# Kernel tuning notes

Hardware: AMD Instinct MI355X
Metric: run time of the kernel (lower is better)

## Reference

```python
import jax, jax.numpy as jnp
import numpy as np

EPS = 1e-5  # torch BatchNorm1d default eps
O, T, D, H1, H2 = 8, 4, 256, 64, 32


def setup_inputs() -> dict:
    key = jax.random.key(0)
    ks = jax.random.split(key, 8)
    B = 65536
    feature = jax.random.normal(ks[0], (B, D), dtype=jnp.float32)
    treatment = jax.random.randint(ks[1], (B,), 0, T, dtype=jnp.int64)
    s1 = 1.0 / np.sqrt(D)
    s2 = 1.0 / np.sqrt(H1)
    s3 = 1.0 / np.sqrt(H2)
    params = {
        # per (outcome, treatment) expert MLP weights
        'W1': jax.random.uniform(ks[2], (O, T, D, H1), jnp.float32, -s1, s1),
        'b1': jnp.zeros((O, T, H1), jnp.float32),
        'g1': jnp.ones((O, T, H1), jnp.float32),   # BN1 gamma
        'be1': jnp.zeros((O, T, H1), jnp.float32),  # BN1 beta
        'm1': jnp.zeros((O, T, H1), jnp.float32),   # BN1 running mean
        'v1': jnp.ones((O, T, H1), jnp.float32),    # BN1 running var
        'W2': jax.random.uniform(ks[3], (O, T, H1, H2), jnp.float32, -s2, s2),
        'b2': jnp.zeros((O, T, H2), jnp.float32),
        'g2': jnp.ones((O, T, H2), jnp.float32),
        'be2': jnp.zeros((O, T, H2), jnp.float32),
        'm2': jnp.zeros((O, T, H2), jnp.float32),
        'v2': jnp.ones((O, T, H2), jnp.float32),
        'W3': jax.random.uniform(ks[4], (O, T, H2), jnp.float32, -s3, s3),  # final Linear(32,1), squeezed
        'b3': jnp.zeros((O, T), jnp.float32),
    }
    return {'feature': feature, 'treatment': treatment, **params}


def _tlearner_fwd(x, t, W1, b1, g1, be1, m1, v1, W2, b2, g2, be2, m2, v2, W3, b3):
    # Dense evaluation of every (outcome, treatment) expert, then per-row
    # selection by treatment id. Equivalent (in eval mode: BN uses running
    # stats, dropout off) to the masked dispatch of the original module.
    h = jnp.einsum('bd,otdh->both', x, W1) + b1          # [B,O,T,H1]
    h = jax.nn.relu(h)
    h = (h - m1) * jax.lax.rsqrt(v1 + EPS) * g1 + be1    # BN1 (eval)
    h = jnp.einsum('both,othk->botk', h, W2) + b2        # [B,O,T,H2]
    h = jax.nn.relu(h)
    h = (h - m2) * jax.lax.rsqrt(v2 + EPS) * g2 + be2    # BN2 (eval)
    out = jnp.einsum('botk,otk->bot', h, W3) + b3        # [B,O,T]
    idx = t.astype(jnp.int32)[:, None, None]             # [B,1,1]
    return jnp.take_along_axis(out, jnp.broadcast_to(idx, (out.shape[0], O, 1)), axis=2)[..., 0]  # [B,O]


def reference(feature, treatment, W1, b1, g1, be1, m1, v1, W2, b2, g2, be2, m2, v2, W3, b3):
    return _tlearner_fwd(feature, treatment, W1, b1, g1, be1, m1, v1,
                         W2, b2, g2, be2, m2, v2, W3, b3)
```

## Files before the change

kernel.cpp:

```cpp
#include <hip/hip_runtime.h>
#include <cstdint>

typedef short bf16x8 __attribute__((ext_vector_type(8)));
typedef float f32x4 __attribute__((ext_vector_type(4)));

#define NO 8
#define NT 4
#define ND 256
#define NH1 64
#define NH2 32
#define BM 64
#define BNEPS 1e-5f

__device__ __forceinline__ unsigned bfpack2(float a, float b) {
    unsigned ua = __float_as_uint(a), ub = __float_as_uint(b);
    ua = (ua + 0x7FFFu + ((ua >> 16) & 1u)) >> 16;
    ub = (ub + 0x7FFFu + ((ub >> 16) & 1u)) >> 16;
    return ua | (ub << 16);
}


__global__ void k_hist_prep(const int* __restrict__ trt, int* __restrict__ ws, int B,
                            const float* __restrict__ W1, const float* __restrict__ W2,
                            const float* __restrict__ b1, const float* __restrict__ g1,
                            const float* __restrict__ be1, const float* __restrict__ m1,
                            const float* __restrict__ v1,
                            const float* __restrict__ b2, const float* __restrict__ g2,
                            const float* __restrict__ be2, const float* __restrict__ m2,
                            const float* __restrict__ v2, const float* __restrict__ W3,
                            unsigned* __restrict__ W1T4, unsigned* __restrict__ W2T4,
                            float* __restrict__ P1, float* __restrict__ P2) {
    const int bid = blockIdx.x, tid = threadIdx.x;
    if (bid < 256) {
        __shared__ int loc[NT];
        if (tid < NT) loc[tid] = 0;
        __syncthreads();
        const int i = bid * 256 + tid;
        if (i < B) atomicAdd(&loc[trt[i] & 3], 1);
        __syncthreads();
        if (tid < NT) atomicAdd(&ws[tid], loc[tid]);
    } else if (bid < 512) {
        const int gi = (bid - 256) * 256 + tid;
        const int lane = gi & 63, nt = (gi >> 6) & 31, c = (gi >> 11) & 7, t = gi >> 14;
        const int n16 = lane & 15, kg = lane >> 4;
        const int n = nt * 16 + n16, o = n >> 6, h = n & 63;
        const int k0 = c * 32 + kg * 8;
        const float* src = W1 + ((size_t)(o * NT + t) * ND + k0) * NH1 + h;
        float v[8];
#pragma unroll
        for (int j = 0; j < 8; ++j) v[j] = src[(size_t)j * NH1];
        uint4 q;
        q.x = bfpack2(v[0], v[1]); q.y = bfpack2(v[2], v[3]);
        q.z = bfpack2(v[4], v[5]); q.w = bfpack2(v[6], v[7]);
        ((uint4*)W1T4)[gi] = q;
    } else if (bid < 544) {
        const int gi = (bid - 512) * 256 + tid;
        const int m16 = gi & 15, kg = (gi >> 4) & 3, ks = (gi >> 6) & 1,
                  kt = (gi >> 7) & 1, o = (gi >> 8) & 7, t = gi >> 11;
        const int k2 = kt * 16 + m16, hb = ks * 32 + kg * 8;
        const float* src = W2 + ((size_t)(o * NT + t) * NH1 + hb) * NH2 + k2;
        float v[8];
#pragma unroll
        for (int j = 0; j < 8; ++j) v[j] = src[(size_t)j * NH2];
        uint4 q;
        q.x = bfpack2(v[0], v[1]); q.y = bfpack2(v[2], v[3]);
        q.z = bfpack2(v[4], v[5]); q.w = bfpack2(v[6], v[7]);
        ((uint4*)W2T4)[gi] = q;
    } else if (bid < 552) {
        const int gi = (bid - 544) * 256 + tid;
        const int t = gi >> 9, n = gi & 511;
        const int o = n >> 6, h = n & 63;
        const int idx = (o * NT + t) * NH1 + h;
        const float sc = g1[idx] * rsqrtf(v1[idx] + BNEPS);
        P1[gi] = sc;
        P1[2048 + gi] = be1[idx] - m1[idx] * sc;
        P1[4096 + gi] = b1[idx];
    } else {
        const int gi = (bid - 552) * 256 + tid;
        const int t = gi >> 8, q = gi & 255;
        const int o = q >> 5, k2 = q & 31;
        const int idx = (o * NT + t) * NH2 + k2;
        const float s = g2[idx] * rsqrtf(v2[idx] + BNEPS);
        const float w3 = W3[idx];
        P2[gi] = s * w3;
        P2[1024 + gi] = (be2[idx] - m2[idx] * s) * w3;
        P2[2048 + gi] = b2[idx];
    }
}

__global__ void k_scatter(const int* __restrict__ trt, int* __restrict__ ws,
                          int* __restrict__ rperm, int B) {
    __shared__ int loc[NT], gb[NT];
    const int tid = threadIdx.x;
    if (tid < NT) loc[tid] = 0;
    __syncthreads();
    const int i = blockIdx.x * blockDim.x + tid;
    int tt = 0, pos = 0;
    if (i < B) { tt = trt[i] & 3; pos = atomicAdd(&loc[tt], 1); }
    __syncthreads();
    if (tid < NT) {
        const int c0 = ws[0], c1 = ws[1], c2 = ws[2];
        const int q0 = (c0 + 63) & ~63, q1 = (c1 + 63) & ~63, q2 = (c2 + 63) & ~63;
        const int eb = tid == 0 ? 0 : tid == 1 ? q0 : tid == 2 ? q0 + q1 : q0 + q1 + q2;
        gb[tid] = eb + atomicAdd(&ws[4 + tid], loc[tid]);
    }
    __syncthreads();
    if (i < B) rperm[gb[tt] + pos] = i;
}

__global__ __launch_bounds__(512, 2) void k_main(
    const float* __restrict__ X, const int* __restrict__ ws, const int* __restrict__ rperm,
    const char* __restrict__ W1T, const char* __restrict__ W2T,
    const float* __restrict__ P1, const float* __restrict__ P2,
    const float* __restrict__ pb3, float* __restrict__ out)
{
    const int c0 = ws[0], c1 = ws[1], c2 = ws[2], c3 = ws[3];
    const int q0 = (c0 + 63) & ~63, q1 = (c1 + 63) & ~63, q2 = (c2 + 63) & ~63;
    const int e0 = q0, e1 = q0 + q1, e2 = e1 + q2, e3 = e2 + ((c3 + 63) & ~63);
    const int m0 = blockIdx.x * BM;
    if (m0 >= e3) return;
    const int t = (m0 >= e0) + (m0 >= e1) + (m0 >= e2);

    const int tid = threadIdx.x;
    const int w = tid >> 6;
    const int l = tid & 63;

    __shared__ __align__(16) char LDS[65536];

    const int rid_l = rperm[m0 + l];

#pragma unroll
    for (int j = 0; j < 8; ++j) {
        const int r = w * 8 + j;
        const int rr = __shfl(rid_l, r);
        const int rrow = rr < 0 ? 0 : rr;
        const float4 xv = *(const float4*)(X + (size_t)rrow * ND + l * 4);
        uint2 pk;
        pk.x = bfpack2(xv.x, xv.y);
        pk.y = bfpack2(xv.z, xv.w);
        *(uint2*)(LDS + r * 512 + ((l * 8) ^ ((r & 7) << 4))) = pk;
    }

    f32x4 acc[4][4];
#pragma unroll
    for (int jn = 0; jn < 4; ++jn)
#pragma unroll
        for (int rt = 0; rt < 4; ++rt) acc[jn][rt] = (f32x4){0.f, 0.f, 0.f, 0.f};

    const char* W1Tw = W1T + (size_t)t * 262144 + (w * 4) * 1024 + l * 16;
    const int ln4 = (l >> 4) * 4;

    __syncthreads();

#pragma unroll
    for (int c = 0; c < 8; ++c) {
        bf16x8 aA[4];
#pragma unroll
        for (int jn = 0; jn < 4; ++jn)
            aA[jn] = *(const bf16x8*)(W1Tw + c * 32768 + jn * 1024);
#pragma unroll
        for (int rt = 0; rt < 4; ++rt) {
            const int r = rt * 16 + (l & 15);
            const bf16x8 bX = *(const bf16x8*)(LDS + r * 512 +
                                               ((c * 64 + (l >> 4) * 16) ^ ((r & 7) << 4)));
#pragma unroll
            for (int jn = 0; jn < 4; ++jn)
                acc[jn][rt] = __builtin_amdgcn_mfma_f32_16x16x32_bf16(aA[jn], bX, acc[jn][rt], 0, 0, 0);
        }
    }
    __syncthreads();

#pragma unroll
    for (int jn = 0; jn < 4; ++jn) {
        const int n0 = (w * 4 + jn) * 16 + ln4;
        const int p = t * 512 + n0;
        const float4 scv = *(const float4*)(P1 + p);
        const float4 shv = *(const float4*)(P1 + 2048 + p);
        const float4 bbv = *(const float4*)(P1 + 4096 + p);
#pragma unroll
        for (int rt = 0; rt < 4; ++rt) {
            const int r = rt * 16 + (l & 15);
            const f32x4 a = acc[jn][rt];
            const float z0 = fmaf(fmaxf(a[0] + bbv.x, 0.f), scv.x, shv.x);
            const float z1 = fmaf(fmaxf(a[1] + bbv.y, 0.f), scv.y, shv.y);
            const float z2 = fmaf(fmaxf(a[2] + bbv.z, 0.f), scv.z, shv.z);
            const float z3 = fmaf(fmaxf(a[3] + bbv.w, 0.f), scv.w, shv.w);
            uint2 pk;
            pk.x = bfpack2(z0, z1); pk.y = bfpack2(z2, z3);
            *(uint2*)(LDS + r * 1024 + (((unsigned)(n0 * 2)) ^ (unsigned)((r & 7) << 4))) = pk;
        }
    }

    bf16x8 aW[2][2];
#pragma unroll
    for (int kt = 0; kt < 2; ++kt)
#pragma unroll
        for (int ks = 0; ks < 2; ++ks)
            aW[kt][ks] = *(const bf16x8*)(W2T +
                ((((size_t)t * NO + w) * 2 + kt) * 2 + ks) * 1024 + l * 16);

    f32x4 acc2[2][4];
#pragma unroll
    for (int kt = 0; kt < 2; ++kt)
#pragma unroll
        for (int rt2 = 0; rt2 < 4; ++rt2) acc2[kt][rt2] = (f32x4){0.f, 0.f, 0.f, 0.f};

#pragma unroll
    for (int rt2 = 0; rt2 < 4; ++rt2) {
        const int r = rt2 * 16 + (l & 15);
        const unsigned swz = (unsigned)((r & 7) << 4);
#pragma unroll
        for (int ks = 0; ks < 2; ++ks) {
            const int n8 = w * 64 + ks * 32 + (l >> 4) * 8;
            const bf16x8 bH = *(const bf16x8*)(LDS + r * 1024 + (((unsigned)(n8 * 2)) ^ swz));
#pragma unroll
            for (int kt = 0; kt < 2; ++kt)
                acc2[kt][rt2] = __builtin_amdgcn_mfma_f32_16x16x32_bf16(aW[kt][ks], bH, acc2[kt][rt2], 0, 0, 0);
        }
    }

    float pr[4];
#pragma unroll
    for (int rt2 = 0; rt2 < 4; ++rt2) pr[rt2] = 0.f;

#pragma unroll
    for (int kt = 0; kt < 2; ++kt) {
        const int q3 = w * 32 + kt * 16 + ln4;
        const int p3 = t * 256 + q3;
        const float4 A3 = *(const float4*)(P2 + p3);
        const float4 C3 = *(const float4*)(P2 + 1024 + p3);
        const float4 bb = *(const float4*)(P2 + 2048 + p3);
#pragma unroll
        for (int rt2 = 0; rt2 < 4; ++rt2) {
            const f32x4 a = acc2[kt][rt2];
            float s = fmaf(fmaxf(a[0] + bb.x, 0.f), A3.x, C3.x);
            s = fmaf(fmaxf(a[1] + bb.y, 0.f), A3.y, s + C3.y);
            s = fmaf(fmaxf(a[2] + bb.z, 0.f), A3.z, s + C3.z);
            s = fmaf(fmaxf(a[3] + bb.w, 0.f), A3.w, s + C3.w);
            pr[rt2] += s;
        }
    }
#pragma unroll
    for (int rt2 = 0; rt2 < 4; ++rt2) {
        float v = pr[rt2];
        v += __shfl_xor(v, 16);
        v += __shfl_xor(v, 32);
        pr[rt2] = v;
    }

    const int sel = l >> 4;
    const float v = sel == 0 ? pr[0] : sel == 1 ? pr[1] : sel == 2 ? pr[2] : pr[3];
    if (rid_l >= 0) out[(size_t)rid_l * NO + w] = v + pb3[w * NT + t];
}

extern "C" void kernel_launch(void* const* d_in, const int* in_sizes, int n_in,
                              void* d_out, int out_size, void* d_ws, size_t ws_size,
                              hipStream_t stream) {
    const float* X   = (const float*)d_in[0];
    const int* trt   = (const int*)d_in[1];
    const float* W1  = (const float*)d_in[2];
    const float* b1  = (const float*)d_in[3];
    const float* g1  = (const float*)d_in[4];
    const float* be1 = (const float*)d_in[5];
    const float* m1  = (const float*)d_in[6];
    const float* v1  = (const float*)d_in[7];
    const float* W2  = (const float*)d_in[8];
    const float* b2  = (const float*)d_in[9];
    const float* g2  = (const float*)d_in[10];
    const float* be2 = (const float*)d_in[11];
    const float* m2  = (const float*)d_in[12];
    const float* v2  = (const float*)d_in[13];
    const float* W3  = (const float*)d_in[14];
    const float* b3  = (const float*)d_in[15];
    float* out = (float*)d_out;

    const int B = in_sizes[1];
    const int permCap = B + 4 * BM;
    int* wsi   = (int*)d_ws;
    int* rperm = wsi + 16;
    char* wsb  = (char*)d_ws;
    size_t off = (64 + (size_t)permCap * 4 + 15) & ~(size_t)15;
    char* W1T = wsb + off;
    char* W2T = W1T + 1048576;
    float* P1 = (float*)(W2T + 131072);
    float* P2 = P1 + 6144;

    hipMemsetAsync(wsi, 0, 64, stream);
    hipMemsetAsync(rperm, 0xFF, (size_t)permCap * 4, stream);

    k_hist_prep<<<556, 256, 0, stream>>>(trt, wsi, B, W1, W2,
                                         b1, g1, be1, m1, v1,
                                         b2, g2, be2, m2, v2, W3,
                                         (unsigned*)W1T, (unsigned*)W2T, P1, P2);
    k_scatter<<<(B + 255) / 256, 256, 0, stream>>>(trt, wsi, rperm, B);

    const int gx = (B + 63) / 64 + 4;
    k_main<<<gx, 512, 0, stream>>>(X, wsi, rperm, W1T, W2T, P1, P2, b3, out);
}
```

Before: 63.18 us.

## Halve row tile to 32, raise occupancy, use hardware bf16 pack

Shrinks the per-block row tile from 64 to 32 rows, which halves LDS use and accumulator registers. This allows launch bounds of 4 blocks per CU instead of 2, and the treatment-group padding and grid size are adjusted to 32-row alignment. The software bf16 rounding is replaced with the v_cvt_pk_bf16_f32 instruction, and the layer-1 bias is folded into the accumulator initialisation. The trade-off is that each block still streams the full per-treatment W1 slice, so total weight traffic from cache roughly doubles.

```diff
diff --git a/kernel.cpp b/kernel.cpp
--- a/kernel.cpp
+++ b/kernel.cpp
@@ -9,7 +9,7 @@
 #define ND 256
 #define NH1 64
 #define NH2 32
-#define BM 64
+#define BM 32
 #define BNEPS 1e-5f
 
 __device__ __forceinline__ unsigned bfpack2(float a, float b) {
@@ -17,6 +17,12 @@
     ua = (ua + 0x7FFFu + ((ua >> 16) & 1u)) >> 16;
     ub = (ub + 0x7FFFu + ((ub >> 16) & 1u)) >> 16;
     return ua | (ub << 16);
+}
+
+__device__ __forceinline__ unsigned cvtpk(float lo, float hi) {
+    unsigned r;
+    asm("v_cvt_pk_bf16_f32 %0, %1, %2" : "=v"(r) : "v"(lo), "v"(hi));
+    return r;
 }
 
 
@@ -100,7 +106,7 @@
     __syncthreads();
     if (tid < NT) {
         const int c0 = ws[0], c1 = ws[1], c2 = ws[2];
-        const int q0 = (c0 + 63) & ~63, q1 = (c1 + 63) & ~63, q2 = (c2 + 63) & ~63;
+        const int q0 = (c0 + 31) & ~31, q1 = (c1 + 31) & ~31, q2 = (c2 + 31) & ~31;
         const int eb = tid == 0 ? 0 : tid == 1 ? q0 : tid == 2 ? q0 + q1 : q0 + q1 + q2;
         gb[tid] = eb + atomicAdd(&ws[4 + tid], loc[tid]);
     }
@@ -108,15 +114,15 @@
     if (i < B) rperm[gb[tt] + pos] = i;
 }
 
-__global__ __launch_bounds__(512, 2) void k_main(
+__global__ __launch_bounds__(512, 4) void k_main(
     const float* __restrict__ X, const int* __restrict__ ws, const int* __restrict__ rperm,
     const char* __restrict__ W1T, const char* __restrict__ W2T,
     const float* __restrict__ P1, const float* __restrict__ P2,
     const float* __restrict__ pb3, float* __restrict__ out)
 {
     const int c0 = ws[0], c1 = ws[1], c2 = ws[2], c3 = ws[3];
-    const int q0 = (c0 + 63) & ~63, q1 = (c1 + 63) & ~63, q2 = (c2 + 63) & ~63;
-    const int e0 = q0, e1 = q0 + q1, e2 = e1 + q2, e3 = e2 + ((c3 + 63) & ~63);
+    const int q0 = (c0 + 31) & ~31, q1 = (c1 + 31) & ~31, q2 = (c2 + 31) & ~31;
+    const int e0 = q0, e1 = q0 + q1, e2 = e1 + q2, e3 = e2 + ((c3 + 31) & ~31);
     const int m0 = blockIdx.x * BM;
     if (m0 >= e3) return;
     const int t = (m0 >= e0) + (m0 >= e1) + (m0 >= e2);
@@ -125,31 +131,34 @@
     const int w = tid >> 6;
     const int l = tid & 63;
 
-    __shared__ __align__(16) char LDS[65536];
-
-    const int rid_l = rperm[m0 + l];
-
-#pragma unroll
-    for (int j = 0; j < 8; ++j) {
-        const int r = w * 8 + j;
-        const int rr = __shfl(rid_l, r);
+    __shared__ __align__(16) char LDS[32768];
+
+    const int rid_o = rperm[m0 + (l & 31)];
+
+#pragma unroll
+    for (int j = 0; j < 4; ++j) {
+        const int r = w * 4 + j;
+        const int rr = __shfl(rid_o, r);
         const int rrow = rr < 0 ? 0 : rr;
         const float4 xv = *(const float4*)(X + (size_t)rrow * ND + l * 4);
         uint2 pk;
-        pk.x = bfpack2(xv.x, xv.y);
-        pk.y = bfpack2(xv.z, xv.w);
+        pk.x = cvtpk(xv.x, xv.y);
+        pk.y = cvtpk(xv.z, xv.w);
         *(uint2*)(LDS + r * 512 + ((l * 8) ^ ((r & 7) << 4))) = pk;
     }
-
-    f32x4 acc[4][4];
-#pragma unroll
-    for (int jn = 0; jn < 4; ++jn)
-#pragma unroll
-        for (int rt = 0; rt < 4; ++rt) acc[jn][rt] = (f32x4){0.f, 0.f, 0.f, 0.f};
 
     const char* W1Tw = W1T + (size_t)t * 262144 + (w * 4) * 1024 + l * 16;
     const int ln4 = (l >> 4) * 4;
 
+    f32x4 acc[4][2];
+#pragma unroll
+    for (int jn = 0; jn < 4; ++jn) {
+        const int n0 = (w * 4 + jn) * 16 + ln4;
+        const float4 bbv = *(const float4*)(P1 + 4096 + t * 512 + n0);
+        acc[jn][0] = (f32x4){bbv.x, bbv.y, bbv.z, bbv.w};
+        acc[jn][1] = acc[jn][0];
+    }
+
     __syncthreads();
 
 #pragma unroll
@@ -159,7 +168,7 @@
         for (int jn = 0; jn < 4; ++jn)
             aA[jn] = *(const bf16x8*)(W1Tw + c * 32768 + jn * 1024);
 #pragma unroll
-        for (int rt = 0; rt < 4; ++rt) {
+        for (int rt = 0; rt < 2; ++rt) {
             const int r = rt * 16 + (l & 15);
             const bf16x8 bX = *(const bf16x8*)(LDS + r * 512 +
                                                ((c * 64 + (l >> 4) * 16) ^ ((r & 7) << 4)));
@@ -176,17 +185,16 @@
         const int p = t * 512 + n0;
         const float4 scv = *(const float4*)(P1 + p);
         const float4 shv = *(const float4*)(P1 + 2048 + p);
-        const float4 bbv = *(const float4*)(P1 + 4096 + p);
-#pragma unroll
-        for (int rt = 0; rt < 4; ++rt) {
+#pragma unroll
+        for (int rt = 0; rt < 2; ++rt) {
             const int r = rt * 16 + (l & 15);
             const f32x4 a = acc[jn][rt];
-            const float z0 = fmaf(fmaxf(a[0] + bbv.x, 0.f), scv.x, shv.x);
-            const float z1 = fmaf(fmaxf(a[1] + bbv.y, 0.f), scv.y, shv.y);
-            const float z2 = fmaf(fmaxf(a[2] + bbv.z, 0.f), scv.z, shv.z);
-            const float z3 = fmaf(fmaxf(a[3] + bbv.w, 0.f), scv.w, shv.w);
+            const float z0 = fmaf(fmaxf(a[0], 0.f), scv.x, shv.x);
+            const float z1 = fmaf(fmaxf(a[1], 0.f), scv.y, shv.y);
+            const float z2 = fmaf(fmaxf(a[2], 0.f), scv.z, shv.z);
+            const float z3 = fmaf(fmaxf(a[3], 0.f), scv.w, shv.w);
             uint2 pk;
-            pk.x = bfpack2(z0, z1); pk.y = bfpack2(z2, z3);
+            pk.x = cvtpk(z0, z1); pk.y = cvtpk(z2, z3);
             *(uint2*)(LDS + r * 1024 + (((unsigned)(n0 * 2)) ^ (unsigned)((r & 7) << 4))) = pk;
         }
     }
@@ -199,14 +207,14 @@
             aW[kt][ks] = *(const bf16x8*)(W2T +
                 ((((size_t)t * NO + w) * 2 + kt) * 2 + ks) * 1024 + l * 16);
 
-    f32x4 acc2[2][4];
+    f32x4 acc2[2][2];
 #pragma unroll
     for (int kt = 0; kt < 2; ++kt)
 #pragma unroll
-        for (int rt2 = 0; rt2 < 4; ++rt2) acc2[kt][rt2] = (f32x4){0.f, 0.f, 0.f, 0.f};
-
-#pragma unroll
-    for (int rt2 = 0; rt2 < 4; ++rt2) {
+        for (int rt2 = 0; rt2 < 2; ++rt2) acc2[kt][rt2] = (f32x4){0.f, 0.f, 0.f, 0.f};
+
+#pragma unroll
+    for (int rt2 = 0; rt2 < 2; ++rt2) {
         const int r = rt2 * 16 + (l & 15);
         const unsigned swz = (unsigned)((r & 7) << 4);
 #pragma unroll
@@ -219,10 +227,7 @@
         }
     }
 
-    float pr[4];
-#pragma unroll
-    for (int rt2 = 0; rt2 < 4; ++rt2) pr[rt2] = 0.f;
-
+    float pr[2] = {0.f, 0.f};
 #pragma unroll
     for (int kt = 0; kt < 2; ++kt) {
         const int q3 = w * 32 + kt * 16 + ln4;
@@ -231,7 +236,7 @@
         const float4 C3 = *(const float4*)(P2 + 1024 + p3);
         const float4 bb = *(const float4*)(P2 + 2048 + p3);
 #pragma unroll
-        for (int rt2 = 0; rt2 < 4; ++rt2) {
+        for (int rt2 = 0; rt2 < 2; ++rt2) {
             const f32x4 a = acc2[kt][rt2];
             float s = fmaf(fmaxf(a[0] + bb.x, 0.f), A3.x, C3.x);
             s = fmaf(fmaxf(a[1] + bb.y, 0.f), A3.y, s + C3.y);
@@ -241,16 +246,17 @@
         }
     }
 #pragma unroll
-    for (int rt2 = 0; rt2 < 4; ++rt2) {
+    for (int rt2 = 0; rt2 < 2; ++rt2) {
         float v = pr[rt2];
         v += __shfl_xor(v, 16);
         v += __shfl_xor(v, 32);
         pr[rt2] = v;
     }
 
-    const int sel = l >> 4;
-    const float v = sel == 0 ? pr[0] : sel == 1 ? pr[1] : sel == 2 ? pr[2] : pr[3];
-    if (rid_l >= 0) out[(size_t)rid_l * NO + w] = v + pb3[w * NT + t];
+    if (l < 32 && rid_o >= 0) {
+        const float v = (l >> 4) ? pr[1] : pr[0];
+        out[(size_t)rid_o * NO + w] = v + pb3[w * NT + t];
+    }
 }
 
 extern "C" void kernel_launch(void* const* d_in, const int* in_sizes, int n_in,
@@ -275,7 +281,7 @@
     float* out = (float*)d_out;
 
     const int B = in_sizes[1];
-    const int permCap = B + 4 * BM;
+    const int permCap = B + 128;
     int* wsi   = (int*)d_ws;
     int* rperm = wsi + 16;
     char* wsb  = (char*)d_ws;
@@ -294,6 +300,6 @@
                                          (unsigned*)W1T, (unsigned*)W2T, P1, P2);
     k_scatter<<<(B + 255) / 256, 256, 0, stream>>>(trt, wsi, rperm, B);
 
-    const int gx = (B + 63) / 64 + 4;
+    const int gx = (B + 128) / 32;
     k_main<<<gx, 512, 0, stream>>>(X, wsi, rperm, W1T, W2T, P1, P2, b3, out);
 }
```

New measurement: 60.86 us. -3.7%, faster.
